# Optimization experiments

Hardware: AMD Instinct MI355X
Metric: run time of the kernel (lower is better)

The kernel has to match this reference:

```python
import jax, jax.numpy as jnp
import numpy as np

B, S, D = 4, 2048, 1024
H, HD = 16, 64  # n_head, head_dim; H*HD == D

def setup_inputs() -> dict:
    key = jax.random.key(0)
    k1, k2, k3 = jax.random.split(key, 3)
    x = jax.random.normal(k1, (B, S, D), dtype=jnp.float32)
    # nn.Linear weights: stored [out, in]; init ~ U(-1/sqrt(in), 1/sqrt(in))
    w_attn = jax.random.uniform(k2, (3 * D, D), dtype=jnp.float32,
                                minval=-1.0, maxval=1.0) / jnp.sqrt(jnp.float32(D))
    w_proj = jax.random.uniform(k3, (D, D), dtype=jnp.float32,
                                minval=-1.0, maxval=1.0) / jnp.sqrt(jnp.float32(D))
    return {"x": x, "w_attn": w_attn, "w_proj": w_proj}

def reference(x, w_attn, w_proj):
    b, s, d = x.shape
    qkv = jnp.einsum('bsd,ed->bse', x, w_attn)              # [b, s, 3D]
    q, k, v = jnp.split(qkv, 3, axis=-1)
    q = q.reshape(b, s, H, HD).transpose(0, 2, 1, 3)        # [b, h, s, hd]
    k = k.reshape(b, s, H, HD).transpose(0, 2, 1, 3)
    v = v.reshape(b, s, H, HD).transpose(0, 2, 1, 3)
    scale = 1.0 / jnp.sqrt(jnp.float32(HD))
    scores = jnp.einsum('bhqd,bhkd->bhqk', q, k) * scale    # [b, h, s, s]
    causal = jnp.tril(jnp.ones((s, s), dtype=bool))
    scores = jnp.where(causal[None, None], scores, -jnp.inf)
    attn = jax.nn.softmax(scores, axis=-1)
    out = jnp.einsum('bhqk,bhkd->bhqd', attn, v)            # [b, h, s, hd]
    out = out.transpose(0, 2, 1, 3).reshape(b, s, d)
    return jnp.einsum('bsd,ed->bse', out, w_proj)
```

## Files before the change

### kernel.cpp

```cpp
#include <hip/hip_runtime.h>
#include <hip/hip_bf16.h>

#define NB   4
#define SEQ  2048
#define DMODEL 1024
#define NHEAD 16
#define HDIM 64
#define MROWS (NB * SEQ)
#define N_QKV (3 * DMODEL)

typedef __attribute__((ext_vector_type(8))) short bf16x8;
typedef __attribute__((ext_vector_type(4))) float f32x4;
typedef __attribute__((ext_vector_type(2))) unsigned int u32x2;

#define MFMA16(a, b, c) __builtin_amdgcn_mfma_f32_16x16x32_bf16((a), (b), (c), 0, 0, 0)

__device__ inline bf16x8 load16(const __hip_bfloat16* p) {
    union { uint4 u; bf16x8 v; } t;
    t.u = *(const uint4*)p;
    return t.v;
}

__device__ inline ushort f2bf(float f) {
    union { float f; unsigned int u; } a;
    a.f = f;
    unsigned int r = a.u + 0x7FFFu + ((a.u >> 16) & 1u);
    return (ushort)(r >> 16);
}

__device__ inline unsigned int cvt_pk_bf16(float lo, float hi) {
    unsigned int r;
    asm("v_cvt_pk_bf16_f32 %0, %1, %2" : "=v"(r) : "v"(lo), "v"(hi));
    return r;
}

__device__ inline void gload_lds16(const __hip_bfloat16* g, __hip_bfloat16* l) {
    __builtin_amdgcn_global_load_lds(
        (const __attribute__((address_space(1))) unsigned int*)g,
        (__attribute__((address_space(3))) unsigned int*)l,
        16, 0, 0);
}

__global__ __launch_bounds__(256)
void cast3_kernel(const float* __restrict__ x, const float* __restrict__ wa,
                  const float* __restrict__ wp, ushort* __restrict__ xb,
                  ushort* __restrict__ wab, ushort* __restrict__ wpb, float qsc) {
    const int bid = (int)blockIdx.x;
    const float* in; ushort* out; int idx; float s = 1.0f;
    if (bid < 8192) {
        in = x;  out = xb;  idx = (bid * 256 + (int)threadIdx.x) * 4;
    } else if (bid < 11264) {
        in = wa; out = wab; idx = ((bid - 8192) * 256 + (int)threadIdx.x) * 4;
        if (idx < DMODEL * DMODEL) s = qsc;
    } else {
        in = wp; out = wpb; idx = ((bid - 11264) * 256 + (int)threadIdx.x) * 4;
    }
    float4 v = *(const float4*)(in + idx);
    ushort4 o;
    o.x = f2bf(v.x * s);
    o.y = f2bf(v.y * s);
    o.z = f2bf(v.z * s);
    o.w = f2bf(v.w * s);
    *(ushort4*)(out + idx) = o;
}

template<int MODE>
__global__ __launch_bounds__(512, 2)
void gemm_bt(const __hip_bfloat16* __restrict__ A,
             const __hip_bfloat16* __restrict__ Bm,
             ushort* __restrict__ Cb,
             float* __restrict__ Cf,
             ushort* __restrict__ Vt,
             int M, int N, int K) {
    constexpr int BM = 256, BN = 128, BK = 64;
    __shared__ __hip_bfloat16 As[3 * BM * BK];
    __shared__ __hip_bfloat16 Bs[3 * BN * BK];

    const int tid  = threadIdx.x;
    const int wave = tid >> 6;
    const int lane = tid & 63;
    const int quad = lane >> 4;
    const int l16  = lane & 15;
    const int wr = (wave >> 1) * 64;
    const int wc = (wave & 1) * 64;
    const int sw8 = l16 & 7;

    const int nbx  = gridDim.x;
    const int nblk = nbx * gridDim.y;
    const int orig = (int)blockIdx.y * nbx + (int)blockIdx.x;
    const int swzb = (orig & 7) * (nblk >> 3) + (orig >> 3);
    const int bx = swzb % nbx, by = swzb / nbx;

    const int row0 = by * BM;
    const int col0 = bx * BN;

    const int srow = tid >> 3;
    const int ssl  = ((tid & 7) ^ ((tid >> 3) & 7)) * 8;
    const __hip_bfloat16* ag = A  + (size_t)(row0 + srow) * K + ssl;
    const __hip_bfloat16* bg = Bm + (size_t)(col0 + srow) * K + ssl;

    auto stageA = [&](int q, int tile, int buf) {
        gload_lds16(ag + (size_t)tile * BK + (size_t)(q * 64) * K,
                    As + buf * 16384 + q * 4096 + wave * 512);
    };
    auto stageB = [&](int q, int tile, int buf) {
        gload_lds16(bg + (size_t)tile * BK + (size_t)(q * 64) * K,
                    Bs + buf * 8192 + q * 4096 + wave * 512);
    };

    f32x4 acc[4][4];
#pragma unroll
    for (int i = 0; i < 4; i++)
#pragma unroll
        for (int j = 0; j < 4; j++) acc[i][j] = (f32x4)0.0f;

#pragma unroll
    for (int q = 0; q < 4; q++) stageA(q, 0, 0);
    stageB(0, 0, 0); stageB(1, 0, 0);
#pragma unroll
    for (int q = 0; q < 4; q++) stageA(q, 1, 1);
    stageB(0, 1, 1); stageB(1, 1, 1);
    asm volatile("s_waitcnt vmcnt(6)" ::: "memory");
    __builtin_amdgcn_s_barrier();
    asm volatile("" ::: "memory");

    const int nk = K / BK;
    int cur = 0;
    for (int t = 0; t < nk; ++t) {
        const bool more = (t + 2 < nk);
        const int nb = (cur + 2 >= 3) ? cur - 1 : cur + 2;
        const __hip_bfloat16* Ab = As + cur * 16384;
        const __hip_bfloat16* Bb = Bs + cur * 8192;

        bf16x8 a0[2][2], bfr[4][2];
#pragma unroll
        for (int i2 = 0; i2 < 2; i2++)
#pragma unroll
            for (int ks = 0; ks < 2; ks++)
                a0[i2][ks] = load16(&Ab[(wr + i2 * 16 + l16) * 64
                                        + (((ks * 4 + quad) ^ sw8) * 8)]);
#pragma unroll
        for (int j = 0; j < 4; j++)
#pragma unroll
            for (int ks = 0; ks < 2; ks++)
                bfr[j][ks] = load16(&Bb[(wc + j * 16 + l16) * 64
                                        + (((ks * 4 + quad) ^ sw8) * 8)]);
        if (more) { stageA(0, t + 2, nb); stageA(1, t + 2, nb); stageB(0, t + 2, nb); }

        __builtin_amdgcn_s_barrier();
        asm volatile("" ::: "memory");
        __builtin_amdgcn_s_setprio(1);
#pragma unroll
        for (int i2 = 0; i2 < 2; i2++)
#pragma unroll
            for (int j = 0; j < 4; j++) {
                acc[i2][j] = MFMA16(a0[i2][0], bfr[j][0], acc[i2][j]);
                acc[i2][j] = MFMA16(a0[i2][1], bfr[j][1], acc[i2][j]);
            }
        __builtin_amdgcn_s_setprio(0);
        __builtin_amdgcn_s_barrier();
        asm volatile("" ::: "memory");

        bf16x8 a1[2][2];
#pragma unroll
        for (int i2 = 0; i2 < 2; i2++)
#pragma unroll
            for (int ks = 0; ks < 2; ks++)
                a1[i2][ks] = load16(&Ab[(wr + 32 + i2 * 16 + l16) * 64
                                        + (((ks * 4 + quad) ^ sw8) * 8)]);
        if (more) { stageA(2, t + 2, nb); stageA(3, t + 2, nb); stageB(1, t + 2, nb); }

        __builtin_amdgcn_s_barrier();
        asm volatile("" ::: "memory");
        __builtin_amdgcn_s_setprio(1);
#pragma unroll
        for (int i2 = 0; i2 < 2; i2++)
#pragma unroll
            for (int j = 0; j < 4; j++) {
                acc[2 + i2][j] = MFMA16(a1[i2][0], bfr[j][0], acc[2 + i2][j]);
                acc[2 + i2][j] = MFMA16(a1[i2][1], bfr[j][1], acc[2 + i2][j]);
            }
        __builtin_amdgcn_s_setprio(0);

        if (more) asm volatile("s_waitcnt vmcnt(6)" ::: "memory");
        else      asm volatile("s_waitcnt vmcnt(0)" ::: "memory");
        __builtin_amdgcn_s_barrier();
        asm volatile("" ::: "memory");

        cur = (cur == 2) ? 0 : cur + 1;
    }

    if constexpr (MODE == 2) {
        if (col0 >= 2 * DMODEL) {
            const int vcol0 = col0 - 2 * DMODEL;
            const int bb = row0 >> 11;
            const int row0m = row0 & 2047;
            const int hh = (vcol0 >> 6) + (wave & 1);
            ushort* Tw = (ushort*)As + wave * 2048;
            ushort* vdst = Vt + ((size_t)(bb * NHEAD + hh) * HDIM) * SEQ;
#pragma unroll
            for (int P = 0; P < 2; P++) {
#pragma unroll
                for (int i2 = 0; i2 < 2; i2++)
#pragma unroll
                    for (int j = 0; j < 4; j++)
#pragma unroll
                        for (int r = 0; r < 4; r++)
                            Tw[(j * 16 + l16) * 32 + i2 * 16 + quad * 4 + r] =
                                f2bf(acc[2 * P + i2][j][r]);
#pragma unroll
                for (int pp = 0; pp < 4; pp++) {
                    int d = pp * 16 + (lane >> 2);
                    int part = lane & 3;
                    uint4 v = *(const uint4*)(Tw + d * 32 + part * 8);
                    *(uint4*)(vdst + (size_t)d * SEQ + row0m + wr + P * 32 + part * 8) = v;
                }
            }
            return;
        }
    }

    ushort* base = nullptr;
    int c0 = 0;
    if constexpr (MODE == 2) {
        base = Cb + ((col0 >= DMODEL) ? (size_t)MROWS * DMODEL : 0);
        c0 = col0 & (DMODEL - 1);
    }
#pragma unroll
    for (int i = 0; i < 4; i++) {
#pragma unroll
        for (int r = 0; r < 4; r++) {
            size_t grow = (size_t)(row0 + wr + i * 16 + quad * 4 + r);
#pragma unroll
            for (int j = 0; j < 4; j++) {
                float v = acc[i][j][r];
                if (MODE == 1) {
                    Cf[grow * N + col0 + wc + j * 16 + l16] = v;
                } else {
                    base[grow * DMODEL + c0 + wc + j * 16 + l16] = f2bf(v);
                }
            }
        }
    }
}

__global__ __launch_bounds__(256)
void attn_kernel(const ushort* __restrict__ Qb, const ushort* __restrict__ Kb,
                 const ushort* __restrict__ Vtb, ushort* __restrict__ O) {
    __shared__ __hip_bfloat16 Kc[4 * 32 * 64];
    __shared__ __hip_bfloat16 Vc[4 * 64 * 32];

    const int tid  = threadIdx.x;
    const int wave = tid >> 6;
    const int lane = tid & 63;
    const int quad = lane >> 4;
    const int l16  = lane & 15;

    const int blk = (int)blockIdx.x;
    const int g   = 15 - (blk >> 6);
    const int bh  = (((blk >> 3) & 7) << 3) | (blk & 7);
    const int b = bh >> 4, h = bh & 15;
    const int p  = 4 * g + wave;
    const int q0 = p * 32;
    const int nc = p + 1;
    const int ncmax = 4 * g + 4;

    bf16x8 ones;
#pragma unroll
    for (int i = 0; i < 8; i++) ones[i] = (short)0x3F80;
    const f32x4 fzero = (f32x4)0.0f;

    bf16x8 qf[2][2];
#pragma unroll
    for (int s = 0; s < 2; s++) {
        const __hip_bfloat16* qp = (const __hip_bfloat16*)Qb
            + ((size_t)b * SEQ + q0 + s * 16 + l16) * DMODEL + h * HDIM;
        qf[s][0] = load16(qp + quad * 8);
        qf[s][1] = load16(qp + 32 + quad * 8);
    }

    const __hip_bfloat16* kbase = (const __hip_bfloat16*)Kb + (size_t)b * SEQ * DMODEL + h * HDIM;
    const __hip_bfloat16* vbase = (const __hip_bfloat16*)Vtb + (size_t)bh * HDIM * SEQ;

    f32x4 oacc[2][4], lacc[2];
#pragma unroll
    for (int s = 0; s < 2; s++) {
        lacc[s] = (f32x4)0.0f;
#pragma unroll
        for (int t = 0; t < 4; t++) oacc[s][t] = (f32x4)0.0f;
    }

    const int slot = wave * 64 + lane;
    const int skey = slot >> 3;
    const int sdsg = (slot & 7) ^ (skey & 7);
    const int svd  = slot >> 2;
    const int svsg = (slot & 3) ^ ((svd >> 1) & 3);
    const __hip_bfloat16* kg = kbase + (size_t)skey * DMODEL + sdsg * 8;
    const __hip_bfloat16* vg = vbase + (size_t)svd * SEQ + svsg * 8;

    auto stage = [&](int buf, int chunk) {
        gload_lds16(kg + (size_t)chunk * (32 * DMODEL), Kc + buf * 2048 + wave * 512);
        gload_lds16(vg + (size_t)chunk * 32,            Vc + buf * 2048 + wave * 512);
    };

    stage(0, 0);
    stage(1, 1);
    asm volatile("s_waitcnt vmcnt(2)" ::: "memory");
    __builtin_amdgcn_s_barrier();
    asm volatile("" ::: "memory");

    const int vswz = (l16 >> 1) & 3;

    for (int cb = 0; cb < ncmax; cb += 4) {
#pragma unroll
        for (int u = 0; u < 4; ++u) {
            const int c = cb + u;
            const bool more = (c + 2 < ncmax);
            if (more) stage((u + 2) & 3, c + 2);

            if (c < nc) {
                const int k0 = c * 32;
                const bool diag = (c == nc - 1);
                const __hip_bfloat16* Kb_l = Kc + u * 2048;
                const __hip_bfloat16* Vb_l = Vc + u * 2048;

                bf16x8 kb[2][2], vb[4];
#pragma unroll
                for (int t = 0; t < 2; t++) {
#pragma unroll
                    for (int hf = 0; hf < 2; hf++)
                        kb[t][hf] = load16(&Kb_l[(t * 16 + l16) * 64
                                                 + (((hf * 4 + quad) ^ (l16 & 7)) * 8)]);
                }
#pragma unroll
                for (int t = 0; t < 4; t++)
                    vb[t] = load16(&Vb_l[(t * 16 + l16) * 32 + ((quad ^ vswz) * 8)]);

#pragma unroll
                for (int s = 0; s < 2; s++) {
                    f32x4 z[2];
#pragma unroll
                    for (int t = 0; t < 2; t++) {
                        f32x4 zz = MFMA16(kb[t][0], qf[s][0], fzero);
                        zz = MFMA16(kb[t][1], qf[s][1], zz);
                        z[t] = zz;
                    }

                    unsigned int xw0, xw1, yw0, yw1;
#pragma unroll
                    for (int t = 0; t < 2; t++) {
                        float e[4];
#pragma unroll
                        for (int r = 0; r < 4; r++) {
                            float sv = z[t][r];
                            if (diag) {
                                int key = k0 + t * 16 + quad * 4 + r;
                                int qq  = q0 + s * 16 + l16;
                                sv = (key <= qq) ? sv : -1e30f;
                            }
                            e[r] = __builtin_amdgcn_exp2f(sv);
                        }
                        unsigned int w0 = cvt_pk_bf16(e[0], e[1]);
                        unsigned int w1 = cvt_pk_bf16(e[2], e[3]);
                        if (t == 0) { xw0 = w0; xw1 = w1; }
                        else        { yw0 = w0; yw1 = w1; }
                    }

                    u32x2 s32_0 = __builtin_amdgcn_permlane32_swap(xw0, yw0, false, false);
                    u32x2 fin_0 = __builtin_amdgcn_permlane16_swap(s32_0.x, s32_0.y, false, false);
                    u32x2 s32_1 = __builtin_amdgcn_permlane32_swap(xw1, yw1, false, false);
                    u32x2 fin_1 = __builtin_amdgcn_permlane16_swap(s32_1.x, s32_1.y, false, false);
                    union { unsigned int u[4]; bf16x8 v; } pk;
                    pk.u[0] = fin_0.x; pk.u[1] = fin_1.x;
                    pk.u[2] = fin_0.y; pk.u[3] = fin_1.y;
                    bf16x8 pa = pk.v;

#pragma unroll
                    for (int t = 0; t < 4; t++)
                        oacc[s][t] = MFMA16(pa, vb[t], oacc[s][t]);
                    lacc[s] = MFMA16(pa, ones, lacc[s]);
                }
            }

            if (more) asm volatile("s_waitcnt vmcnt(2)" ::: "memory");
            else      asm volatile("s_waitcnt vmcnt(0)" ::: "memory");
            __builtin_amdgcn_s_barrier();
            asm volatile("" ::: "memory");
        }
    }

#pragma unroll
    for (int s = 0; s < 2; s++) {
        float inv[4];
#pragma unroll
        for (int r = 0; r < 4; r++) inv[r] = 1.0f / lacc[s][r];
#pragma unroll
        for (int t = 0; t < 4; t++) {
#pragma unroll
            for (int r = 0; r < 4; r++) {
                float v = oacc[s][t][r] * inv[r];
                O[((size_t)b * SEQ + q0 + s * 16 + quad * 4 + r) * DMODEL
                  + h * HDIM + t * 16 + l16] = f2bf(v);
            }
        }
    }
}

extern "C" void kernel_launch(void* const* d_in, const int* in_sizes, int n_in,
                              void* d_out, int out_size, void* d_ws, size_t ws_size,
                              hipStream_t stream) {
    const float* x      = (const float*)d_in[0];
    const float* w_attn = (const float*)d_in[1];
    const float* w_proj = (const float*)d_in[2];
    float* out = (float*)d_out;

    ushort* ws   = (ushort*)d_ws;
    ushort* xb   = ws;
    ushort* wab  = xb  + (size_t)MROWS * DMODEL;
    ushort* wpb  = wab + (size_t)N_QKV * DMODEL;
    ushort* qkvb = wpb + (size_t)DMODEL * DMODEL;
    ushort* ob   = qkvb + (size_t)MROWS * N_QKV;

    ushort* qreg = qkvb;
    ushort* kreg = qkvb + (size_t)MROWS * DMODEL;
    ushort* vtreg = qkvb + 2 * (size_t)MROWS * DMODEL;

    const float qsc = 0.125f * 1.44269504f;

    cast3_kernel<<<12288, 256, 0, stream>>>(x, w_attn, w_proj, xb, wab, wpb, qsc);

    gemm_bt<2><<<dim3(N_QKV / 128, MROWS / 256), 512, 0, stream>>>(
        (const __hip_bfloat16*)xb, (const __hip_bfloat16*)wab, qreg, nullptr, vtreg,
        MROWS, N_QKV, DMODEL);

    attn_kernel<<<1024, 256, 0, stream>>>(qreg, kreg, vtreg, ob);

    gemm_bt<1><<<dim3(DMODEL / 128, MROWS / 256), 512, 0, stream>>>(
        (const __hip_bfloat16*)ob, (const __hip_bfloat16*)wpb, nullptr, out, nullptr,
        MROWS, DMODEL, DMODEL);
}
```

Baseline: 232.8 us.

## Enlarge GEMM tile to 256x256 with double-buffered staging

The bf16 GEMM block tile grows from 256x128 to 256x256. Each wave now computes a 128x64 sub-tile over four MFMA phases, and the LDS pipeline moves from triple to double buffering with reordered interleaved loads. The goal is more operand reuse per LDS load and less global traffic per output. In exchange it doubles the accumulator registers, which may hurt occupancy, and halves the grid size, which could leave CUs underused on the smaller projection GEMM (128 blocks).

```diff
diff --git a/kernel.cpp b/kernel.cpp
--- a/kernel.cpp
+++ b/kernel.cpp
@@ -72,17 +72,17 @@
              float* __restrict__ Cf,
              ushort* __restrict__ Vt,
              int M, int N, int K) {
-    constexpr int BM = 256, BN = 128, BK = 64;
-    __shared__ __hip_bfloat16 As[3 * BM * BK];
-    __shared__ __hip_bfloat16 Bs[3 * BN * BK];
+    constexpr int BM = 256, BN = 256, BK = 64;
+    __shared__ __hip_bfloat16 As[2 * BM * BK];
+    __shared__ __hip_bfloat16 Bs[2 * BN * BK];
 
     const int tid  = threadIdx.x;
     const int wave = tid >> 6;
     const int lane = tid & 63;
     const int quad = lane >> 4;
     const int l16  = lane & 15;
-    const int wr = (wave >> 1) * 64;
-    const int wc = (wave & 1) * 64;
+    const int wr = (wave >> 2) * 128;
+    const int wc = (wave & 3) * 64;
     const int sw8 = l16 & 7;
 
     const int nbx  = gridDim.x;
@@ -105,48 +105,48 @@
     };
     auto stageB = [&](int q, int tile, int buf) {
         gload_lds16(bg + (size_t)tile * BK + (size_t)(q * 64) * K,
-                    Bs + buf * 8192 + q * 4096 + wave * 512);
+                    Bs + buf * 16384 + q * 4096 + wave * 512);
     };
 
-    f32x4 acc[4][4];
-#pragma unroll
-    for (int i = 0; i < 4; i++)
+    f32x4 acc[8][4];
+#pragma unroll
+    for (int i = 0; i < 8; i++)
 #pragma unroll
         for (int j = 0; j < 4; j++) acc[i][j] = (f32x4)0.0f;
 
 #pragma unroll
-    for (int q = 0; q < 4; q++) stageA(q, 0, 0);
-    stageB(0, 0, 0); stageB(1, 0, 0);
-#pragma unroll
-    for (int q = 0; q < 4; q++) stageA(q, 1, 1);
-    stageB(0, 1, 1); stageB(1, 1, 1);
+    for (int q = 0; q < 4; q++) stageB(q, 0, 0);
+    stageA(0, 0, 0); stageA(2, 0, 0); stageA(1, 0, 0); stageA(3, 0, 0);
+#pragma unroll
+    for (int q = 0; q < 4; q++) stageB(q, 1, 1);
+    stageA(0, 1, 1); stageA(2, 1, 1);
     asm volatile("s_waitcnt vmcnt(6)" ::: "memory");
     __builtin_amdgcn_s_barrier();
     asm volatile("" ::: "memory");
 
     const int nk = K / BK;
-    int cur = 0;
     for (int t = 0; t < nk; ++t) {
-        const bool more = (t + 2 < nk);
-        const int nb = (cur + 2 >= 3) ? cur - 1 : cur + 2;
+        const int cur = t & 1;
+        const int nxt = cur ^ 1;
         const __hip_bfloat16* Ab = As + cur * 16384;
-        const __hip_bfloat16* Bb = Bs + cur * 8192;
-
-        bf16x8 a0[2][2], bfr[4][2];
-#pragma unroll
-        for (int i2 = 0; i2 < 2; i2++)
-#pragma unroll
-            for (int ks = 0; ks < 2; ks++)
-                a0[i2][ks] = load16(&Ab[(wr + i2 * 16 + l16) * 64
-                                        + (((ks * 4 + quad) ^ sw8) * 8)]);
+        const __hip_bfloat16* Bb = Bs + cur * 16384;
+        const bool p1 = (t + 1 < nk), p2 = (t + 2 < nk);
+
+        bf16x8 bfr[4][2], af[2][2];
+
 #pragma unroll
         for (int j = 0; j < 4; j++)
 #pragma unroll
             for (int ks = 0; ks < 2; ks++)
                 bfr[j][ks] = load16(&Bb[(wc + j * 16 + l16) * 64
                                         + (((ks * 4 + quad) ^ sw8) * 8)]);
-        if (more) { stageA(0, t + 2, nb); stageA(1, t + 2, nb); stageB(0, t + 2, nb); }
-
+#pragma unroll
+        for (int i2 = 0; i2 < 2; i2++)
+#pragma unroll
+            for (int ks = 0; ks < 2; ks++)
+                af[i2][ks] = load16(&Ab[(wr + i2 * 16 + l16) * 64
+                                        + (((ks * 4 + quad) ^ sw8) * 8)]);
+        if (p1) { stageA(1, t + 1, nxt); stageA(3, t + 1, nxt); }
         __builtin_amdgcn_s_barrier();
         asm volatile("" ::: "memory");
         __builtin_amdgcn_s_setprio(1);
@@ -154,22 +154,22 @@
         for (int i2 = 0; i2 < 2; i2++)
 #pragma unroll
             for (int j = 0; j < 4; j++) {
-                acc[i2][j] = MFMA16(a0[i2][0], bfr[j][0], acc[i2][j]);
-                acc[i2][j] = MFMA16(a0[i2][1], bfr[j][1], acc[i2][j]);
+                acc[i2][j] = MFMA16(af[i2][0], bfr[j][0], acc[i2][j]);
+                acc[i2][j] = MFMA16(af[i2][1], bfr[j][1], acc[i2][j]);
             }
         __builtin_amdgcn_s_setprio(0);
         __builtin_amdgcn_s_barrier();
         asm volatile("" ::: "memory");
 
-        bf16x8 a1[2][2];
 #pragma unroll
         for (int i2 = 0; i2 < 2; i2++)
 #pragma unroll
             for (int ks = 0; ks < 2; ks++)
-                a1[i2][ks] = load16(&Ab[(wr + 32 + i2 * 16 + l16) * 64
+                af[i2][ks] = load16(&Ab[(wr + 32 + i2 * 16 + l16) * 64
                                         + (((ks * 4 + quad) ^ sw8) * 8)]);
-        if (more) { stageA(2, t + 2, nb); stageA(3, t + 2, nb); stageB(1, t + 2, nb); }
-
+        if (p2) { stageB(0, t + 2, cur); stageB(1, t + 2, cur); }
+        if (p2) asm volatile("s_waitcnt vmcnt(10)" ::: "memory");
+        else    asm volatile("s_waitcnt vmcnt(0)"  ::: "memory");
         __builtin_amdgcn_s_barrier();
         asm volatile("" ::: "memory");
         __builtin_amdgcn_s_setprio(1);
@@ -177,29 +177,71 @@
         for (int i2 = 0; i2 < 2; i2++)
 #pragma unroll
             for (int j = 0; j < 4; j++) {
-                acc[2 + i2][j] = MFMA16(a1[i2][0], bfr[j][0], acc[2 + i2][j]);
-                acc[2 + i2][j] = MFMA16(a1[i2][1], bfr[j][1], acc[2 + i2][j]);
+                acc[2 + i2][j] = MFMA16(af[i2][0], bfr[j][0], acc[2 + i2][j]);
+                acc[2 + i2][j] = MFMA16(af[i2][1], bfr[j][1], acc[2 + i2][j]);
             }
         __builtin_amdgcn_s_setprio(0);
-
-        if (more) asm volatile("s_waitcnt vmcnt(6)" ::: "memory");
-        else      asm volatile("s_waitcnt vmcnt(0)" ::: "memory");
-        __builtin_amdgcn_s_barrier();
-        asm volatile("" ::: "memory");
-
-        cur = (cur == 2) ? 0 : cur + 1;
-    }
+        __builtin_amdgcn_s_barrier();
+        asm volatile("" ::: "memory");
+
+#pragma unroll
+        for (int i2 = 0; i2 < 2; i2++)
+#pragma unroll
+            for (int ks = 0; ks < 2; ks++)
+                af[i2][ks] = load16(&Ab[(wr + 64 + i2 * 16 + l16) * 64
+                                        + (((ks * 4 + quad) ^ sw8) * 8)]);
+        if (p2) { stageB(2, t + 2, cur); stageB(3, t + 2, cur); }
+        __builtin_amdgcn_s_barrier();
+        asm volatile("" ::: "memory");
+        __builtin_amdgcn_s_setprio(1);
+#pragma unroll
+        for (int i2 = 0; i2 < 2; i2++)
+#pragma unroll
+            for (int j = 0; j < 4; j++) {
+                acc[4 + i2][j] = MFMA16(af[i2][0], bfr[j][0], acc[4 + i2][j]);
+                acc[4 + i2][j] = MFMA16(af[i2][1], bfr[j][1], acc[4 + i2][j]);
+            }
+        __builtin_amdgcn_s_setprio(0);
+        __builtin_amdgcn_s_barrier();
+        asm volatile("" ::: "memory");
+
+#pragma unroll
+        for (int i2 = 0; i2 < 2; i2++)
+#pragma unroll
+            for (int ks = 0; ks < 2; ks++)
+                af[i2][ks] = load16(&Ab[(wr + 96 + i2 * 16 + l16) * 64
+                                        + (((ks * 4 + quad) ^ sw8) * 8)]);
+        if (p2) { stageA(0, t + 2, cur); stageA(2, t + 2, cur); }
+        if (p2) asm volatile("s_waitcnt vmcnt(8)" ::: "memory");
+        else    asm volatile("s_waitcnt vmcnt(0)" ::: "memory");
+        __builtin_amdgcn_s_barrier();
+        asm volatile("" ::: "memory");
+        __builtin_amdgcn_s_setprio(1);
+#pragma unroll
+        for (int i2 = 0; i2 < 2; i2++)
+#pragma unroll
+            for (int j = 0; j < 4; j++) {
+                acc[6 + i2][j] = MFMA16(af[i2][0], bfr[j][0], acc[6 + i2][j]);
+                acc[6 + i2][j] = MFMA16(af[i2][1], bfr[j][1], acc[6 + i2][j]);
+            }
+        __builtin_amdgcn_s_setprio(0);
+        __builtin_amdgcn_s_barrier();
+        asm volatile("" ::: "memory");
+    }
+    asm volatile("s_waitcnt vmcnt(0)" ::: "memory");
+    __builtin_amdgcn_s_barrier();
+    asm volatile("" ::: "memory");
 
     if constexpr (MODE == 2) {
         if (col0 >= 2 * DMODEL) {
             const int vcol0 = col0 - 2 * DMODEL;
             const int bb = row0 >> 11;
             const int row0m = row0 & 2047;
-            const int hh = (vcol0 >> 6) + (wave & 1);
+            const int hh = (vcol0 >> 6) + (wave & 3);
             ushort* Tw = (ushort*)As + wave * 2048;
             ushort* vdst = Vt + ((size_t)(bb * NHEAD + hh) * HDIM) * SEQ;
 #pragma unroll
-            for (int P = 0; P < 2; P++) {
+            for (int P = 0; P < 4; P++) {
 #pragma unroll
                 for (int i2 = 0; i2 < 2; i2++)
 #pragma unroll
@@ -227,7 +269,7 @@
         c0 = col0 & (DMODEL - 1);
     }
 #pragma unroll
-    for (int i = 0; i < 4; i++) {
+    for (int i = 0; i < 8; i++) {
 #pragma unroll
         for (int r = 0; r < 4; r++) {
             size_t grow = (size_t)(row0 + wr + i * 16 + quad * 4 + r);
@@ -429,13 +471,13 @@
 
     cast3_kernel<<<12288, 256, 0, stream>>>(x, w_attn, w_proj, xb, wab, wpb, qsc);
 
-    gemm_bt<2><<<dim3(N_QKV / 128, MROWS / 256), 512, 0, stream>>>(
+    gemm_bt<2><<<dim3(N_QKV / 256, MROWS / 256), 512, 0, stream>>>(
         (const __hip_bfloat16*)xb, (const __hip_bfloat16*)wab, qreg, nullptr, vtreg,
         MROWS, N_QKV, DMODEL);
 
     attn_kernel<<<1024, 256, 0, stream>>>(qreg, kreg, vtreg, ob);
 
-    gemm_bt<1><<<dim3(DMODEL / 128, MROWS / 256), 512, 0, stream>>>(
+    gemm_bt<1><<<dim3(DMODEL / 256, MROWS / 256), 512, 0, stream>>>(
         (const __hip_bfloat16*)ob, (const __hip_bfloat16*)wpb, nullptr, out, nullptr,
         MROWS, DMODEL, DMODEL);
 }
```

Result: slower. 249.9 us (+7.3%).
